# Kernel optimization log

Measured on AMD Instinct MI355X. Metric: run time of the kernel, lower is better.

## Reference

```python
import jax, jax.numpy as jnp
import numpy as np

PICK_WIN = 20      # int(round(pick_win_s / dt)) = int(round(2.0 / 0.1))
W_PICK = 0.1
BETA = 25.0


def setup_inputs() -> dict:
    key = jax.random.key(0)
    k1, k2 = jax.random.split(key)
    B, T = 4096, 6000
    pred = jax.random.normal(k1, (B, T), dtype=jnp.float32)
    target = jax.random.normal(k2, (B, T), dtype=jnp.float32)
    return {"pred": pred, "target": target}


def _windowed_soft_argmax(x, mask, pos):
    # soft_argmax(|x[s:e]|, beta) + s  ==  sum_j softmax(beta*|x_j| over j in [s,e)) * j
    logits = jnp.where(mask, BETA * jnp.abs(x), -jnp.inf)  # [B, T]
    p = jax.nn.softmax(logits, axis=-1)
    return jnp.sum(p * pos.astype(x.dtype), axis=-1)       # [B]


def reference(pred, target):
    loss = jnp.mean(jnp.abs(pred - target))  # nn.L1Loss (mean)

    T = target.shape[-1]
    center = jnp.argmax(jnp.abs(target), axis=-1)          # [B]
    pos = jnp.arange(T)                                     # [T]
    # window [max(0, c-W), min(T, c+W)) expressed as a mask over absolute positions
    mask = (pos[None, :] >= center[:, None] - PICK_WIN) & (pos[None, :] < center[:, None] + PICK_WIN)

    picks_pred = _windowed_soft_argmax(pred, mask, pos)
    picks_true = _windowed_soft_argmax(target, mask, pos)

    pick_loss = jnp.mean(jnp.abs(picks_pred - picks_true)) / T
    return loss + W_PICK * pick_loss
```

## Files before the change

### kernel.cpp

```cpp
#include <hip/hip_runtime.h>
#include <math.h>

#define T_LEN 6000
#define B_ROWS 4096
#define PICK_WIN 20
#define BETA 25.0f

__global__ __launch_bounds__(256) void row_pass1(const float* __restrict__ pred,
                                                 const float* __restrict__ target,
                                                 float* __restrict__ row_l1,
                                                 int* __restrict__ row_center) {
    const int row = blockIdx.x;
    const int tid = threadIdx.x;
    const float4* p4 = (const float4*)(pred + (size_t)row * T_LEN);
    const float4* t4 = (const float4*)(target + (size_t)row * T_LEN);

    float sum = 0.0f;
    float bestv = -1.0f;
    int   besti = 0x7fffffff;

    for (int i = tid; i < T_LEN / 4; i += 256) {
        float4 p = p4[i];
        float4 t = t4[i];
        sum += fabsf(p.x - t.x) + fabsf(p.y - t.y) +
               fabsf(p.z - t.z) + fabsf(p.w - t.w);
        const int base = i * 4;
        float a;
        a = fabsf(t.x); if (a > bestv) { bestv = a; besti = base;     }
        a = fabsf(t.y); if (a > bestv) { bestv = a; besti = base + 1; }
        a = fabsf(t.z); if (a > bestv) { bestv = a; besti = base + 2; }
        a = fabsf(t.w); if (a > bestv) { bestv = a; besti = base + 3; }
    }

    __shared__ float s_sum[256];
    __shared__ float s_val[256];
    __shared__ int   s_idx[256];
    s_sum[tid] = sum; s_val[tid] = bestv; s_idx[tid] = besti;
    __syncthreads();

    for (int off = 128; off > 0; off >>= 1) {
        if (tid < off) {
            s_sum[tid] += s_sum[tid + off];
            const float v  = s_val[tid + off];
            const int   ix = s_idx[tid + off];
            if (v > s_val[tid] || (v == s_val[tid] && ix < s_idx[tid])) {
                s_val[tid] = v; s_idx[tid] = ix;
            }
        }
        __syncthreads();
    }

    if (tid == 0) {
        row_l1[row]     = s_sum[0];
        row_center[row] = s_idx[0];
    }
}

__global__ __launch_bounds__(256) void pick_pass(const float* __restrict__ pred,
                                                 const float* __restrict__ target,
                                                 const int* __restrict__ row_center,
                                                 float* __restrict__ row_pick) {
    const int row  = blockIdx.x * 4 + (threadIdx.x >> 6);
    const int lane = threadIdx.x & 63;

    const int c = row_center[row];
    const int s = max(0, c - PICK_WIN);
    const int e = min(T_LEN, c + PICK_WIN);
    const int len = e - s;

    float ap = -INFINITY, at = -INFINITY;
    const float posf = (float)(s + lane);
    if (lane < len) {
        const size_t idx = (size_t)row * T_LEN + s + lane;
        ap = BETA * fabsf(pred[idx]);
        at = BETA * fabsf(target[idx]);
    }

    float mp = ap, mt = at;
    #pragma unroll
    for (int o = 32; o > 0; o >>= 1) {
        mp = fmaxf(mp, __shfl_xor(mp, o));
        mt = fmaxf(mt, __shfl_xor(mt, o));
    }

    float wp = 0.0f, wt = 0.0f, wpp = 0.0f, wtp = 0.0f;
    if (lane < len) {
        wp  = expf(ap - mp);
        wt  = expf(at - mt);
        wpp = wp * posf;
        wtp = wt * posf;
    }
    #pragma unroll
    for (int o = 32; o > 0; o >>= 1) {
        wp  += __shfl_xor(wp,  o);
        wt  += __shfl_xor(wt,  o);
        wpp += __shfl_xor(wpp, o);
        wtp += __shfl_xor(wtp, o);
    }

    if (lane == 0) {
        row_pick[row] = fabsf(wpp / wp - wtp / wt);
    }
}

__global__ __launch_bounds__(256) void finalize(const float* __restrict__ row_l1,
                                                const float* __restrict__ row_pick,
                                                float* __restrict__ out) {
    __shared__ float s1[256], s2[256];
    const int tid = threadIdx.x;
    float a = 0.0f, b = 0.0f;
    for (int i = tid; i < B_ROWS; i += 256) {
        a += row_l1[i];
        b += row_pick[i];
    }
    s1[tid] = a; s2[tid] = b;
    __syncthreads();
    for (int off = 128; off > 0; off >>= 1) {
        if (tid < off) { s1[tid] += s1[tid + off]; s2[tid] += s2[tid + off]; }
        __syncthreads();
    }
    if (tid == 0) {
        const float loss = s1[0] / (float)((long long)B_ROWS * (long long)T_LEN);
        const float pick = (s2[0] / (float)B_ROWS) / (float)T_LEN;
        out[0] = loss + 0.1f * pick;
    }
}

extern "C" void kernel_launch(void* const* d_in, const int* in_sizes, int n_in,
                              void* d_out, int out_size, void* d_ws, size_t ws_size,
                              hipStream_t stream) {
    const float* pred   = (const float*)d_in[0];
    const float* target = (const float*)d_in[1];
    float* out = (float*)d_out;

    float* row_l1     = (float*)d_ws;
    int*   row_center = (int*)(row_l1 + B_ROWS);
    float* row_pick   = (float*)(row_center + B_ROWS);

    row_pass1<<<B_ROWS, 256, 0, stream>>>(pred, target, row_l1, row_center);
    pick_pass<<<B_ROWS / 4, 256, 0, stream>>>(pred, target, row_center, row_pick);
    finalize<<<1, 256, 0, stream>>>(row_l1, row_pick, out);
}
```

Before: 43.64 us.

## Fuse windowed soft-argmax into row reduction kernel and preload row into registers

Moves the windowed soft-argmax computation into the first per-row kernel, so the first wavefront handles it right after the block reduction finds the argmax center. This drops a kernel launch and the round trip of the centers through global memory. The row is also loaded up front into register arrays of six float4 per tensor, so all loads are issued before any compute. In exchange, the pick step runs serially at the tail of each block and register pressure goes up.

Result: faster. 40.23 us (-7.8%).

```diff
diff --git a/kernel.cpp b/kernel.cpp
--- a/kernel.cpp
+++ b/kernel.cpp
@@ -9,27 +9,39 @@
 __global__ __launch_bounds__(256) void row_pass1(const float* __restrict__ pred,
                                                  const float* __restrict__ target,
                                                  float* __restrict__ row_l1,
-                                                 int* __restrict__ row_center) {
+                                                 float* __restrict__ row_pick) {
     const int row = blockIdx.x;
     const int tid = threadIdx.x;
-    const float4* p4 = (const float4*)(pred + (size_t)row * T_LEN);
-    const float4* t4 = (const float4*)(target + (size_t)row * T_LEN);
+    const float4* __restrict__ p4 = (const float4*)(pred + (size_t)row * T_LEN);
+    const float4* __restrict__ t4 = (const float4*)(target + (size_t)row * T_LEN);
+
+    float4 p[6], t[6];
+    const int  i5   = tid + 5 * 256;
+    const bool has6 = (i5 < T_LEN / 4);
+
+    #pragma unroll
+    for (int k = 0; k < 5; ++k) {
+        p[k] = p4[tid + k * 256];
+        t[k] = t4[tid + k * 256];
+    }
+    if (has6) { p[5] = p4[i5]; t[5] = t4[i5]; }
 
     float sum = 0.0f;
     float bestv = -1.0f;
     int   besti = 0x7fffffff;
 
-    for (int i = tid; i < T_LEN / 4; i += 256) {
-        float4 p = p4[i];
-        float4 t = t4[i];
-        sum += fabsf(p.x - t.x) + fabsf(p.y - t.y) +
-               fabsf(p.z - t.z) + fabsf(p.w - t.w);
-        const int base = i * 4;
+    #pragma unroll
+    for (int k = 0; k < 6; ++k) {
+        if (k == 5 && !has6) break;
+        const int base = (tid + k * 256) * 4;
+        const float4 pp = p[k], tt = t[k];
+        sum += fabsf(pp.x - tt.x) + fabsf(pp.y - tt.y) +
+               fabsf(pp.z - tt.z) + fabsf(pp.w - tt.w);
         float a;
-        a = fabsf(t.x); if (a > bestv) { bestv = a; besti = base;     }
-        a = fabsf(t.y); if (a > bestv) { bestv = a; besti = base + 1; }
-        a = fabsf(t.z); if (a > bestv) { bestv = a; besti = base + 2; }
-        a = fabsf(t.w); if (a > bestv) { bestv = a; besti = base + 3; }
+        a = fabsf(tt.x); if (a > bestv) { bestv = a; besti = base;     }
+        a = fabsf(tt.y); if (a > bestv) { bestv = a; besti = base + 1; }
+        a = fabsf(tt.z); if (a > bestv) { bestv = a; besti = base + 2; }
+        a = fabsf(tt.w); if (a > bestv) { bestv = a; besti = base + 3; }
     }
 
     __shared__ float s_sum[256];
@@ -50,56 +62,46 @@
         __syncthreads();
     }
 
-    if (tid == 0) {
-        row_l1[row]     = s_sum[0];
-        row_center[row] = s_idx[0];
-    }
-}
+    if (tid < 64) {
+        const int c   = s_idx[0];
+        const int s   = max(0, c - PICK_WIN);
+        const int e   = min(T_LEN, c + PICK_WIN);
+        const int len = e - s;
 
-__global__ __launch_bounds__(256) void pick_pass(const float* __restrict__ pred,
-                                                 const float* __restrict__ target,
-                                                 const int* __restrict__ row_center,
-                                                 float* __restrict__ row_pick) {
-    const int row  = blockIdx.x * 4 + (threadIdx.x >> 6);
-    const int lane = threadIdx.x & 63;
+        float ap = -INFINITY, at = -INFINITY;
+        const float posf = (float)(s + tid);
+        if (tid < len) {
+            const size_t idx = (size_t)row * T_LEN + s + tid;
+            ap = BETA * fabsf(pred[idx]);
+            at = BETA * fabsf(target[idx]);
+        }
 
-    const int c = row_center[row];
-    const int s = max(0, c - PICK_WIN);
-    const int e = min(T_LEN, c + PICK_WIN);
-    const int len = e - s;
+        float mp = ap, mt = at;
+        #pragma unroll
+        for (int o = 32; o > 0; o >>= 1) {
+            mp = fmaxf(mp, __shfl_xor(mp, o));
+            mt = fmaxf(mt, __shfl_xor(mt, o));
+        }
 
-    float ap = -INFINITY, at = -INFINITY;
-    const float posf = (float)(s + lane);
-    if (lane < len) {
-        const size_t idx = (size_t)row * T_LEN + s + lane;
-        ap = BETA * fabsf(pred[idx]);
-        at = BETA * fabsf(target[idx]);
-    }
+        float wp = 0.0f, wt = 0.0f, wpp = 0.0f, wtp = 0.0f;
+        if (tid < len) {
+            wp  = expf(ap - mp);
+            wt  = expf(at - mt);
+            wpp = wp * posf;
+            wtp = wt * posf;
+        }
+        #pragma unroll
+        for (int o = 32; o > 0; o >>= 1) {
+            wp  += __shfl_xor(wp,  o);
+            wt  += __shfl_xor(wt,  o);
+            wpp += __shfl_xor(wpp, o);
+            wtp += __shfl_xor(wtp, o);
+        }
 
-    float mp = ap, mt = at;
-    #pragma unroll
-    for (int o = 32; o > 0; o >>= 1) {
-        mp = fmaxf(mp, __shfl_xor(mp, o));
-        mt = fmaxf(mt, __shfl_xor(mt, o));
-    }
-
-    float wp = 0.0f, wt = 0.0f, wpp = 0.0f, wtp = 0.0f;
-    if (lane < len) {
-        wp  = expf(ap - mp);
-        wt  = expf(at - mt);
-        wpp = wp * posf;
-        wtp = wt * posf;
-    }
-    #pragma unroll
-    for (int o = 32; o > 0; o >>= 1) {
-        wp  += __shfl_xor(wp,  o);
-        wt  += __shfl_xor(wt,  o);
-        wpp += __shfl_xor(wpp, o);
-        wtp += __shfl_xor(wtp, o);
-    }
-
-    if (lane == 0) {
-        row_pick[row] = fabsf(wpp / wp - wtp / wt);
+        if (tid == 0) {
+            row_l1[row]   = s_sum[0];
+            row_pick[row] = fabsf(wpp / wp - wtp / wt);
+        }
     }
 }
 
@@ -133,11 +135,9 @@
     const float* target = (const float*)d_in[1];
     float* out = (float*)d_out;
 
-    float* row_l1     = (float*)d_ws;
-    int*   row_center = (int*)(row_l1 + B_ROWS);
-    float* row_pick   = (float*)(row_center + B_ROWS);
+    float* row_l1   = (float*)d_ws;
+    float* row_pick = row_l1 + B_ROWS;
 
-    row_pass1<<<B_ROWS, 256, 0, stream>>>(pred, target, row_l1, row_center);
-    pick_pass<<<B_ROWS / 4, 256, 0, stream>>>(pred, target, row_center, row_pick);
+    row_pass1<<<B_ROWS, 256, 0, stream>>>(pred, target, row_l1, row_pick);
     finalize<<<1, 256, 0, stream>>>(row_l1, row_pick, out);
 }
```
